# Performance work log

Hardware: AMD Instinct MI355X
Metric: run time of the kernel (lower is better)

Reference implementation:

```python
import jax, jax.numpy as jnp
import numpy as np
import math

B, S, D, H = 4, 2048, 1024, 16
DK = D // H  # 64


def setup_inputs() -> dict:
    key = jax.random.key(0)
    ks = jax.random.split(key, 8)
    sc = 1.0 / math.sqrt(D)
    Q = jax.random.normal(ks[0], (B, S, D), dtype=jnp.float32)
    K = jax.random.normal(ks[1], (B, S, D), dtype=jnp.float32)
    V = jax.random.normal(ks[2], (B, S, D), dtype=jnp.float32)
    # per-head projection weights, stacked: [H, D, DK]
    Wq = jax.random.normal(ks[3], (H, D, DK), dtype=jnp.float32) * sc
    Wk = jax.random.normal(ks[4], (H, D, DK), dtype=jnp.float32) * sc
    Wv = jax.random.normal(ks[5], (H, D, DK), dtype=jnp.float32) * sc
    Wo = jax.random.normal(ks[6], (D, D), dtype=jnp.float32) * sc
    bo = jax.random.normal(ks[7], (D,), dtype=jnp.float32) * sc
    mask = jnp.tril(jnp.ones((S, S), dtype=bool))  # causal
    return {"Q": Q, "K": K, "V": V, "mask": mask,
            "Wq": Wq, "Wk": Wk, "Wv": Wv, "Wo": Wo, "bo": bo}


def reference(Q, K, V, mask, Wq, Wk, Wv, Wo, bo):
    # batched per-head projections: [B,S,D] x [H,D,DK] -> [B,H,S,DK]
    q = jnp.einsum('bsd,hdk->bhsk', Q, Wq)
    k = jnp.einsum('bsd,hdk->bhsk', K, Wk)
    v = jnp.einsum('bsd,hdk->bhsk', V, Wv)
    # NOTE: source scales by k.shape[-1]/sqrt(d_k) = d_k/sqrt(d_k) = sqrt(d_k)
    scale = jnp.float32(DK / math.sqrt(DK))
    w = jnp.einsum('bhsk,bhtk->bhst', q, k) * scale  # [B,H,S,S]
    w = jnp.where(mask[None, None, :, :], w, jnp.float32(-jnp.inf))
    w = jax.nn.softmax(w, axis=-1)
    out = jnp.einsum('bhst,bhtk->bhsk', w, v)  # [B,H,S,DK]
    # concat heads along last dim (head order preserved): [B,S,D]
    concat = out.transpose(0, 2, 1, 3).reshape(B, S, D)
    # output projection (dropout p=0 -> identity in eval)
    return concat @ Wo.T + bo
```

## Files before the change

kernel.cpp:

```cpp
#include <hip/hip_runtime.h>
#include <math.h>


#define BB 4
#define SS 2048
#define DD 1024
#define HH 16
#define DKK 64
#define MM (BB * SS)

typedef unsigned short u16;
typedef _Float16 f16x8 __attribute__((ext_vector_type(8)));
typedef float f32x4 __attribute__((ext_vector_type(4)));
typedef __attribute__((address_space(1))) unsigned int gas_u32;
typedef __attribute__((address_space(3))) unsigned int las_u32;

__device__ __forceinline__ float bf2f(u16 u) {
    union { unsigned int i; float f; } c;
    c.i = ((unsigned int)u) << 16;
    return c.f;
}
__device__ __forceinline__ u16 f2h(float f) {
    _Float16 h = (_Float16)f;
    return __builtin_bit_cast(u16, h);
}
__device__ __forceinline__ void split1(float x, u16& hi, u16& lo) {
    _Float16 hh = (_Float16)x;
    hi = __builtin_bit_cast(u16, hh);
    lo = f2h(x - (float)hh);
}
__device__ __forceinline__ void gld16(const void* g, void* l) {
    __builtin_amdgcn_global_load_lds((gas_u32*)g, (las_u32*)l, 16, 0, 0);
}

__global__ void sniff_kernel(const u16* t0, const u16* t1, const u16* t2,
                             const u16* t3, const u16* t4, const u16* t5,
                             const u16* t6, const u16* t7, int* flags)
{
    const u16* ptrs[8] = {t0, t1, t2, t3, t4, t5, t6, t7};
    const u16* p = ptrs[blockIdx.x];
    int tid = threadIdx.x;
    int cnt = 0;
    #pragma unroll
    for (int i = 0; i < 8; i++) {
        u16 v = p[tid * 8 + i];
        int e = (v >> 7) & 0xFF;
        if (e >= 0xF0 || (e <= 0x0F && (v & 0x7FFF) != 0)) cnt++;
    }
    #pragma unroll
    for (int off = 32; off; off >>= 1) cnt += __shfl_down(cnt, off);
    if (tid == 0) flags[blockIdx.x] = (cnt >= 4) ? 1 : 0;
}

__global__ __launch_bounds__(256) void split_x_kernel(
    const void* __restrict__ X, const int* __restrict__ flags, int fidx,
    u16* __restrict__ Xh, u16* __restrict__ Xl)
{
    const int xf = flags[fidx];
    size_t idx = ((size_t)blockIdx.x * 256 + threadIdx.x) * 8;
    float x[8];
    if (xf) {
        float4 a = *(const float4*)((const float*)X + idx);
        float4 b = *(const float4*)((const float*)X + idx + 4);
        x[0] = a.x; x[1] = a.y; x[2] = a.z; x[3] = a.w;
        x[4] = b.x; x[5] = b.y; x[6] = b.z; x[7] = b.w;
    } else {
        ushort4 a = *(const ushort4*)((const u16*)X + idx);
        ushort4 b = *(const ushort4*)((const u16*)X + idx + 4);
        x[0] = bf2f(a.x); x[1] = bf2f(a.y); x[2] = bf2f(a.z); x[3] = bf2f(a.w);
        x[4] = bf2f(b.x); x[5] = bf2f(b.y); x[6] = bf2f(b.z); x[7] = bf2f(b.w);
    }
    union { u16 u[8]; uint4 v; } H, L;
    #pragma unroll
    for (int i = 0; i < 8; i++) split1(x[i], H.u[i], L.u[i]);
    *(uint4*)(Xh + idx) = H.v;
    *(uint4*)(Xl + idx) = L.v;
}

__global__ __launch_bounds__(256) void split_wqkv_kernel(
    const void* __restrict__ Wq, const void* __restrict__ Wk, const void* __restrict__ Wv,
    const int* __restrict__ flags, u16* __restrict__ Wth, u16* __restrict__ Wtl)
{
    const int z = blockIdx.z, h = blockIdx.y, kc = blockIdx.x;
    const void* __restrict__ W = (z == 0) ? Wq : (z == 1) ? Wk : Wv;
    const int wf = flags[3 + z];
    __shared__ float T[64][65];
    const int t = threadIdx.x;
    {
        const int kk = t >> 2, ns = (t & 3) * 16;
        const size_t base = (size_t)h * DD * DKK + (size_t)(kc * 64 + kk) * DKK + ns;
        #pragma unroll
        for (int j = 0; j < 4; j++) {
            if (wf) {
                float4 v = *(const float4*)((const float*)W + base + 4 * j);
                T[kk][ns + 4 * j + 0] = v.x; T[kk][ns + 4 * j + 1] = v.y;
                T[kk][ns + 4 * j + 2] = v.z; T[kk][ns + 4 * j + 3] = v.w;
            } else {
                ushort4 v = *(const ushort4*)((const u16*)W + base + 4 * j);
                T[kk][ns + 4 * j + 0] = bf2f(v.x); T[kk][ns + 4 * j + 1] = bf2f(v.y);
                T[kk][ns + 4 * j + 2] = bf2f(v.z); T[kk][ns + 4 * j + 3] = bf2f(v.w);
            }
        }
    }
    __syncthreads();
    {
        const int n = t >> 2, ks = (t & 3) * 16;
        union { u16 u[16]; uint4 v[2]; } Hv, Lv;
        #pragma unroll
        for (int i = 0; i < 16; i++) split1(T[ks + i][n], Hv.u[i], Lv.u[i]);
        size_t ob = ((size_t)(z * HH + h) * DKK + n) * DD + kc * 64 + ks;
        *(uint4*)(Wth + ob)     = Hv.v[0];
        *(uint4*)(Wth + ob + 8) = Hv.v[1];
        *(uint4*)(Wtl + ob)     = Lv.v[0];
        *(uint4*)(Wtl + ob + 8) = Lv.v[1];
    }
}

__global__ __launch_bounds__(256, 4) void proj_v4_kernel(
    const void* __restrict__ Q, const void* __restrict__ K, const void* __restrict__ V,
    const u16* __restrict__ Wth, const u16* __restrict__ Wtl,
    const int* __restrict__ flags,
    u16* __restrict__ qb, u16* __restrict__ kb, u16* __restrict__ vb)
{
    const int z = blockIdx.z;
    const void* __restrict__ X = (z == 0) ? Q : (z == 1) ? K : V;
    u16* __restrict__ out      = (z == 0) ? qb : (z == 1) ? kb : vb;
    const int xf = flags[z];
    const int h0 = blockIdx.y * 2;
    const int m0 = blockIdx.x * 128;

    __shared__ __align__(16) u16 WH[128 * 64];
    __shared__ __align__(16) u16 WL[128 * 64];

    const int tid  = threadIdx.x;
    const int lane = tid & 63, wave = tid >> 6;
    const int quad = lane >> 4, ln = lane & 15;

    const int lr = lane >> 3, lg = (lane & 7) ^ (lane >> 3);
    const size_t wsrc0 = ((size_t)((z * HH + h0) * DKK) + wave * 32 + lr) * DD + lg * 8;
    const size_t arow = (size_t)(m0 + wave * 32 + ln) * DD + quad * 8;

    f32x4 acc[2][8];
    #pragma unroll
    for (int mh = 0; mh < 2; mh++)
        #pragma unroll
        for (int nt = 0; nt < 8; nt++)
            acc[mh][nt] = (f32x4){0.f, 0.f, 0.f, 0.f};

    for (int kbase = 0; kbase < DD; kbase += 64) {
        __syncthreads();
        f16x8 a_h[2][2], a_l[2][2];
        #pragma unroll
        for (int kh = 0; kh < 2; kh++)
            #pragma unroll
            for (int mh = 0; mh < 2; mh++) {
                size_t o = arow + (size_t)(mh * 16) * DD + kbase + kh * 32;
                float x[8];
                if (xf) {
                    float4 a = *(const float4*)((const float*)X + o);
                    float4 b = *(const float4*)((const float*)X + o + 4);
                    x[0] = a.x; x[1] = a.y; x[2] = a.z; x[3] = a.w;
                    x[4] = b.x; x[5] = b.y; x[6] = b.z; x[7] = b.w;
                } else {
                    ushort4 a = *(const ushort4*)((const u16*)X + o);
                    ushort4 b = *(const ushort4*)((const u16*)X + o + 4);
                    x[0] = bf2f(a.x); x[1] = bf2f(a.y); x[2] = bf2f(a.z); x[3] = bf2f(a.w);
                    x[4] = bf2f(b.x); x[5] = bf2f(b.y); x[6] = bf2f(b.z); x[7] = bf2f(b.w);
                }
                union { u16 u[8]; f16x8 v; } H, L;
                #pragma unroll
                for (int i = 0; i < 8; i++) split1(x[i], H.u[i], L.u[i]);
                a_h[kh][mh] = H.v;
                a_l[kh][mh] = L.v;
            }
        #pragma unroll
        for (int j = 0; j < 4; j++) {
            gld16(Wth + wsrc0 + (size_t)j * 8 * DD + kbase, &WH[(wave * 32 + j * 8) * 64]);
            gld16(Wtl + wsrc0 + (size_t)j * 8 * DD + kbase, &WL[(wave * 32 + j * 8) * 64]);
        }
        asm volatile("s_waitcnt vmcnt(0)" ::: "memory");
        __syncthreads();

        #pragma unroll
        for (int kh = 0; kh < 2; kh++) {
            const int kg = ((kh * 4 + quad) ^ (ln & 7)) * 8;
            #pragma unroll
            for (int nt = 0; nt < 8; nt++) {
                const int n = nt * 16 + ln;
                f16x8 bh = __builtin_bit_cast(f16x8, *(const uint4*)&WH[n * 64 + kg]);
                f16x8 bl = __builtin_bit_cast(f16x8, *(const uint4*)&WL[n * 64 + kg]);
                #pragma unroll
                for (int mh = 0; mh < 2; mh++) {
                    acc[mh][nt] = __builtin_amdgcn_mfma_f32_16x16x32_f16(a_l[kh][mh], bh, acc[mh][nt], 0, 0, 0);
                    acc[mh][nt] = __builtin_amdgcn_mfma_f32_16x16x32_f16(a_h[kh][mh], bl, acc[mh][nt], 0, 0, 0);
                    acc[mh][nt] = __builtin_amdgcn_mfma_f32_16x16x32_f16(a_h[kh][mh], bh, acc[mh][nt], 0, 0, 0);
                }
            }
        }
    }

    #pragma unroll
    for (int mh = 0; mh < 2; mh++)
        #pragma unroll
        for (int r = 0; r < 4; r++) {
            int m = m0 + wave * 32 + mh * 16 + quad * 4 + r;
            int b = m >> 11, s = m & 2047;
            #pragma unroll
            for (int nt = 0; nt < 8; nt++) {
                int head = h0 + (nt >> 2);
                u16* op = out + (((size_t)(b * HH + head) * SS + s)) * DKK;
                op[(nt & 3) * 16 + ln] = f2h(acc[mh][nt][r]);
            }
        }
}

__global__ __launch_bounds__(512) void attn_kernel(
    const u16* __restrict__ qb, const u16* __restrict__ kb,
    const u16* __restrict__ vb, u16* __restrict__ cath, u16* __restrict__ catl)
{
    __shared__ __align__(16) u16 Kt[2][64 * 64];
    __shared__ __align__(16) u16 Vt[2][64 * 64];
    __shared__ __align__(16) u16 Pw[8][16 * 64];

    const int tid  = threadIdx.x;
    const int lane = tid & 63, wave = tid >> 6;
    const int quad = lane >> 4, ln = lane & 15;

    const int p  = blockIdx.x;
    const int bh = (p >> 6) * 8 + (p & 7);
    const int pairidx = (p >> 3) & 7;
    const int b = bh >> 4, h = bh & 15;

    const int skey = tid >> 3, kgrp = tid & 7;
    const int koff = skey * 64 + ((kgrp ^ (skey & 7)) << 3);
    const int vkey = tid & 63, vdkb = (tid >> 6) * 8;

    const u16* kbp = kb + (size_t)bh * SS * DKK;
    const u16* vbp = vb + (size_t)bh * SS * DKK;

    #pragma unroll 1
    for (int half = 0; half < 2; half++) {
        const int xt = half == 0 ? 15 - pairidx : pairidx;
        const int qbase = xt * 128;
        const int ktmax = 2 * xt + 1;

        const int wq = qbase + wave * 16;
        const int diagkt = wq >> 6;
        const int wqmax = wq + 15;

        const u16* qp = qb + ((size_t)bh * SS + wq + ln) * DKK;
        f16x8 qf0 = __builtin_bit_cast(f16x8, *(const uint4*)(qp + quad * 8));
        f16x8 qf1 = __builtin_bit_cast(f16x8, *(const uint4*)(qp + 32 + quad * 8));

        f32x4 acc[4];
        #pragma unroll
        for (int n = 0; n < 4; n++) acc[n] = (f32x4){0.f, 0.f, 0.f, 0.f};
        float mrow[4], lrow[4];
        #pragma unroll
        for (int r = 0; r < 4; r++) { mrow[r] = -INFINITY; lrow[r] = 0.f; }

        {
            uint4 ka = *(const uint4*)(kbp + (size_t)skey * DKK + kgrp * 8);
            uint4 va = *(const uint4*)(vbp + (size_t)vkey * DKK + vdkb);
            *(uint4*)&Kt[0][koff] = ka;
            u16 vv[8];
            *(uint4*)&vv[0] = va;
            #pragma unroll
            for (int i = 0; i < 8; i++) {
                int row = vdkb + i;
                Vt[0][row * 64 + (((vkey >> 3) ^ (row & 7)) << 3) + (vkey & 7)] = vv[i];
            }
        }
        __syncthreads();

        int cur = 0;
        for (int kt = 0; kt <= ktmax; ++kt) {
            uint4 ka, va;
            const bool pfb = (kt < ktmax);
            if (pfb) {
                ka = *(const uint4*)(kbp + (size_t)((kt + 1) * 64 + skey) * DKK + kgrp * 8);
                va = *(const uint4*)(vbp + (size_t)((kt + 1) * 64 + vkey) * DKK + vdkb);
            }

            if (kt * 64 <= wqmax) {
                const u16* KT = Kt[cur];
                const u16* VT = Vt[cur];
                f32x4 sa[4];
                #pragma unroll
                for (int n = 0; n < 4; n++) {
                    sa[n] = (f32x4){0.f, 0.f, 0.f, 0.f};
                    const int krow = n * 16 + ln;
                    f16x8 kf0 = __builtin_bit_cast(f16x8,
                        *(const uint4*)&KT[krow * 64 + ((quad ^ (ln & 7)) << 3)]);
                    sa[n] = __builtin_amdgcn_mfma_f32_16x16x32_f16(qf0, kf0, sa[n], 0, 0, 0);
                    f16x8 kf1 = __builtin_bit_cast(f16x8,
                        *(const uint4*)&KT[krow * 64 + (((quad + 4) ^ (ln & 7)) << 3)]);
                    sa[n] = __builtin_amdgcn_mfma_f32_16x16x32_f16(qf1, kf1, sa[n], 0, 0, 0);
                }

                float sc[4][4];
                const bool diag = (kt == diagkt);
                #pragma unroll
                for (int n = 0; n < 4; n++)
                    #pragma unroll
                    for (int r = 0; r < 4; r++) {
                        float s = sa[n][r] * 8.0f;
                        if (diag && (kt * 64 + n * 16 + ln) > (wq + quad * 4 + r))
                            s = -INFINITY;
                        sc[n][r] = s;
                    }

                float rmax[4];
                #pragma unroll
                for (int r = 0; r < 4; r++)
                    rmax[r] = fmaxf(fmaxf(sc[0][r], sc[1][r]), fmaxf(sc[2][r], sc[3][r]));
                #pragma unroll
                for (int off = 1; off < 16; off <<= 1)
                    #pragma unroll
                    for (int r = 0; r < 4; r++)
                        rmax[r] = fmaxf(rmax[r], __shfl_xor(rmax[r], off));
                float alpha[4];
                #pragma unroll
                for (int r = 0; r < 4; r++) {
                    float mn = fmaxf(mrow[r], rmax[r]);
                    alpha[r] = __expf(mrow[r] - mn);
                    mrow[r] = mn;
                }
                u16* pw = Pw[wave];
                float lsum[4] = {0.f, 0.f, 0.f, 0.f};
                #pragma unroll
                for (int n = 0; n < 4; n++)
                    #pragma unroll
                    for (int r = 0; r < 4; r++) {
                        float pp = __expf(sc[n][r] - mrow[r]);
                        _Float16 ph = (_Float16)pp;
                        const int row = quad * 4 + r;
                        pw[row * 64 + (((n * 2 + (ln >> 3)) ^ (row & 7)) << 3) + (ln & 7)]
                            = __builtin_bit_cast(u16, ph);
                        lsum[r] += (float)ph;
                    }
                #pragma unroll
                for (int off = 1; off < 16; off <<= 1)
                    #pragma unroll
                    for (int r = 0; r < 4; r++)
                        lsum[r] += __shfl_xor(lsum[r], off);
                #pragma unroll
                for (int r = 0; r < 4; r++)
                    lrow[r] = lrow[r] * alpha[r] + lsum[r];
                #pragma unroll
                for (int n = 0; n < 4; n++)
                    #pragma unroll
                    for (int r = 0; r < 4; r++)
                        acc[n][r] *= alpha[r];

                asm volatile("s_waitcnt lgkmcnt(0)" ::: "memory");
                f16x8 pf0 = __builtin_bit_cast(f16x8,
                    *(const uint4*)&pw[ln * 64 + ((quad ^ (ln & 7)) << 3)]);
                f16x8 pf1 = __builtin_bit_cast(f16x8,
                    *(const uint4*)&pw[ln * 64 + (((quad + 4) ^ (ln & 7)) << 3)]);

                #pragma unroll
                for (int n = 0; n < 4; n++) {
                    const int vrow = n * 16 + ln;
                    f16x8 vf0 = __builtin_bit_cast(f16x8,
                        *(const uint4*)&VT[vrow * 64 + ((quad ^ (ln & 7)) << 3)]);
                    acc[n] = __builtin_amdgcn_mfma_f32_16x16x32_f16(pf0, vf0, acc[n], 0, 0, 0);
                    f16x8 vf1 = __builtin_bit_cast(f16x8,
                        *(const uint4*)&VT[vrow * 64 + (((quad + 4) ^ (ln & 7)) << 3)]);
                    acc[n] = __builtin_amdgcn_mfma_f32_16x16x32_f16(pf1, vf1, acc[n], 0, 0, 0);
                }
            }

            if (pfb) {
                *(uint4*)&Kt[cur ^ 1][koff] = ka;
                u16 vv[8];
                *(uint4*)&vv[0] = va;
                #pragma unroll
                for (int i = 0; i < 8; i++) {
                    int row = vdkb + i;
                    Vt[cur ^ 1][row * 64 + (((vkey >> 3) ^ (row & 7)) << 3) + (vkey & 7)] = vv[i];
                }
            }
            __syncthreads();
            cur ^= 1;
        }

        #pragma unroll
        for (int r = 0; r < 4; r++) {
            float inv = 1.0f / lrow[r];
            int row = wq + quad * 4 + r;
            size_t o = ((size_t)b * SS + row) * DD + h * DKK;
            #pragma unroll
            for (int n = 0; n < 4; n++) {
                float v = acc[n][r] * inv;
                u16 hh, ll;
                split1(v, hh, ll);
                cath[o + n * 16 + ln] = hh;
                catl[o + n * 16 + ln] = ll;
            }
        }
    }
}

__global__ __launch_bounds__(256, 4) void outproj_v3_kernel(
    const u16* __restrict__ Ah, const u16* __restrict__ Al,
    const u16* __restrict__ Woh, const u16* __restrict__ Wol,
    const void* __restrict__ bo, const int* __restrict__ flags,
    float* __restrict__ out)
{
    const int n0 = blockIdx.y * 128;
    const int m0 = blockIdx.x * 128;

    __shared__ __align__(16) u16 WH[128 * 64];
    __shared__ __align__(16) u16 WL[128 * 64];

    const int tid  = threadIdx.x;
    const int lane = tid & 63, wave = tid >> 6;
    const int quad = lane >> 4, ln = lane & 15;

    const int lr = lane >> 3, lg = (lane & 7) ^ (lane >> 3);
    const size_t wsrc0 = ((size_t)(n0 + wave * 32 + lr)) * DD + lg * 8;
    const size_t arow  = (size_t)(m0 + wave * 32 + ln) * DD + quad * 8;

    f32x4 acc[2][8];
    #pragma unroll
    for (int mh = 0; mh < 2; mh++)
        #pragma unroll
        for (int nt = 0; nt < 8; nt++)
            acc[mh][nt] = (f32x4){0.f, 0.f, 0.f, 0.f};

    for (int kbase = 0; kbase < DD; kbase += 64) {
        __syncthreads();
        f16x8 a_h[2][2], a_l[2][2];
        #pragma unroll
        for (int kh = 0; kh < 2; kh++)
            #pragma unroll
            for (int mh = 0; mh < 2; mh++) {
                size_t o = arow + (size_t)(mh * 16) * DD + kbase + kh * 32;
                a_h[kh][mh] = __builtin_bit_cast(f16x8, *(const uint4*)(Ah + o));
                a_l[kh][mh] = __builtin_bit_cast(f16x8, *(const uint4*)(Al + o));
            }
        #pragma unroll
        for (int j = 0; j < 4; j++) {
            gld16(Woh + wsrc0 + (size_t)j * 8 * DD + kbase, &WH[(wave * 32 + j * 8) * 64]);
            gld16(Wol + wsrc0 + (size_t)j * 8 * DD + kbase, &WL[(wave * 32 + j * 8) * 64]);
        }
        asm volatile("s_waitcnt vmcnt(0)" ::: "memory");
        __syncthreads();

        #pragma unroll
        for (int kh = 0; kh < 2; kh++) {
            const int kg = ((kh * 4 + quad) ^ (ln & 7)) * 8;
            #pragma unroll
            for (int nt = 0; nt < 8; nt++) {
                const int n = nt * 16 + ln;
                f16x8 bh = __builtin_bit_cast(f16x8, *(const uint4*)&WH[n * 64 + kg]);
                f16x8 bl = __builtin_bit_cast(f16x8, *(const uint4*)&WL[n * 64 + kg]);
                #pragma unroll
                for (int mh = 0; mh < 2; mh++) {
                    acc[mh][nt] = __builtin_amdgcn_mfma_f32_16x16x32_f16(a_l[kh][mh], bh, acc[mh][nt], 0, 0, 0);
                    acc[mh][nt] = __builtin_amdgcn_mfma_f32_16x16x32_f16(a_h[kh][mh], bl, acc[mh][nt], 0, 0, 0);
                    acc[mh][nt] = __builtin_amdgcn_mfma_f32_16x16x32_f16(a_h[kh][mh], bh, acc[mh][nt], 0, 0, 0);
                }
            }
        }
    }

    const int bf = flags[7];
    float bias[8];
    #pragma unroll
    for (int nt = 0; nt < 8; nt++) {
        int n = n0 + nt * 16 + ln;
        bias[nt] = bf ? ((const float*)bo)[n] : bf2f(((const u16*)bo)[n]);
    }
    #pragma unroll
    for (int mh = 0; mh < 2; mh++)
        #pragma unroll
        for (int r = 0; r < 4; r++) {
            int m = m0 + wave * 32 + mh * 16 + quad * 4 + r;
            float* op = out + (size_t)m * DD + n0;
            #pragma unroll
            for (int nt = 0; nt < 8; nt++)
                op[nt * 16 + ln] = acc[mh][nt][r] + bias[nt];
        }
}

extern "C" void kernel_launch(void* const* d_in, const int* in_sizes, int n_in,
                              void* d_out, int out_size, void* d_ws, size_t ws_size,
                              hipStream_t stream)
{
    const void* Q = d_in[0];
    const void* K = d_in[1];
    const void* V = d_in[2];
    const int widx = (n_in >= 9) ? 4 : 3;
    const void* Wq = d_in[widx + 0];
    const void* Wk = d_in[widx + 1];
    const void* Wv = d_in[widx + 2];
    const void* Wo = d_in[widx + 3];
    const void* bo = d_in[widx + 4];
    float* out = (float*)d_out;

    const size_t per = (size_t)BB * HH * SS * DKK;
    u16* qb = (u16*)d_ws;
    u16* kb = qb + per;
    u16* vb = kb + per;
    u16* cath = vb + per;
    u16* catl = cath + per;
    const size_t wtn = (size_t)3 * HH * DKK * DD;
    u16* Wth = catl + per;
    u16* Wtl = Wth + wtn;
    u16* Woh = Wtl + wtn;
    u16* Wol = Woh + (size_t)DD * DD;
    int* flags = (int*)(Wol + (size_t)DD * DD);

    sniff_kernel<<<8, 64, 0, stream>>>(
        (const u16*)Q, (const u16*)K, (const u16*)V,
        (const u16*)Wq, (const u16*)Wk, (const u16*)Wv,
        (const u16*)Wo, (const u16*)bo, flags);

    split_wqkv_kernel<<<dim3(DD / 64, HH, 3), 256, 0, stream>>>(
        Wq, Wk, Wv, flags, Wth, Wtl);
    split_x_kernel<<<(DD * DD) / 2048, 256, 0, stream>>>(Wo, flags, 6, Woh, Wol);

    proj_v4_kernel<<<dim3(MM / 128, HH / 2, 3), 256, 0, stream>>>(
        Q, K, V, Wth, Wtl, flags, qb, kb, vb);

    attn_kernel<<<(SS / 256) * BB * HH, 512, 0, stream>>>(qb, kb, vb, cath, catl);

    outproj_v3_kernel<<<dim3(MM / 128, DD / 128), 256, 0, stream>>>(
        cath, catl, Woh, Wol, bo, flags, out);
}
```

Measured before the change: 470.6 us.

## Double-buffer weight tiles and prefetch A operands in projection GEMMs

The QKV projection and output projection kernels now use double-buffered LDS tiles for the weight halves. The next k-step's A-operand global loads and weight async copies are issued before the current step's MFMA work, so memory latency overlaps with compute. The MFMA section runs at raised wave priority via s_setprio. LDS use per block doubles and launch bounds drop to 2 blocks per CU. That lowers occupancy and adds register pressure from the prefetched A registers.

Result: no change. 478.9 us (+1.8%).

```diff
diff --git a/kernel.cpp b/kernel.cpp
--- a/kernel.cpp
+++ b/kernel.cpp
@@ -116,7 +116,7 @@
     }
 }
 
-__global__ __launch_bounds__(256, 4) void proj_v4_kernel(
+__global__ __launch_bounds__(256, 2) void proj_v5_kernel(
     const void* __restrict__ Q, const void* __restrict__ K, const void* __restrict__ V,
     const u16* __restrict__ Wth, const u16* __restrict__ Wtl,
     const int* __restrict__ flags,
@@ -129,8 +129,8 @@
     const int h0 = blockIdx.y * 2;
     const int m0 = blockIdx.x * 128;
 
-    __shared__ __align__(16) u16 WH[128 * 64];
-    __shared__ __align__(16) u16 WL[128 * 64];
+    __shared__ __align__(16) u16 WH[2][128 * 64];
+    __shared__ __align__(16) u16 WL[2][128 * 64];
 
     const int tid  = threadIdx.x;
     const int lane = tid & 63, wave = tid >> 6;
@@ -147,25 +147,38 @@
         for (int nt = 0; nt < 8; nt++)
             acc[mh][nt] = (f32x4){0.f, 0.f, 0.f, 0.f};
 
-    for (int kbase = 0; kbase < DD; kbase += 64) {
-        __syncthreads();
-        f16x8 a_h[2][2], a_l[2][2];
+    uint4 ra[2][2], rb[2][2];
+    f16x8 a_h[2][2], a_l[2][2];
+
+    auto issueA = [&](int kbase) {
         #pragma unroll
         for (int kh = 0; kh < 2; kh++)
             #pragma unroll
             for (int mh = 0; mh < 2; mh++) {
                 size_t o = arow + (size_t)(mh * 16) * DD + kbase + kh * 32;
+                if (xf) {
+                    ra[kh][mh] = *(const uint4*)((const float*)X + o);
+                    rb[kh][mh] = *(const uint4*)((const float*)X + o + 4);
+                } else {
+                    ra[kh][mh] = *(const uint4*)((const u16*)X + o);
+                }
+            }
+    };
+    auto splitA = [&]() {
+        #pragma unroll
+        for (int kh = 0; kh < 2; kh++)
+            #pragma unroll
+            for (int mh = 0; mh < 2; mh++) {
                 float x[8];
                 if (xf) {
-                    float4 a = *(const float4*)((const float*)X + o);
-                    float4 b = *(const float4*)((const float*)X + o + 4);
+                    float4 a = __builtin_bit_cast(float4, ra[kh][mh]);
+                    float4 b = __builtin_bit_cast(float4, rb[kh][mh]);
                     x[0] = a.x; x[1] = a.y; x[2] = a.z; x[3] = a.w;
                     x[4] = b.x; x[5] = b.y; x[6] = b.z; x[7] = b.w;
                 } else {
-                    ushort4 a = *(const ushort4*)((const u16*)X + o);
-                    ushort4 b = *(const ushort4*)((const u16*)X + o + 4);
-                    x[0] = bf2f(a.x); x[1] = bf2f(a.y); x[2] = bf2f(a.z); x[3] = bf2f(a.w);
-                    x[4] = bf2f(b.x); x[5] = bf2f(b.y); x[6] = bf2f(b.z); x[7] = bf2f(b.w);
+                    union { uint4 v; u16 u[8]; } c; c.v = ra[kh][mh];
+                    #pragma unroll
+                    for (int i = 0; i < 8; i++) x[i] = bf2f(c.u[i]);
                 }
                 union { u16 u[8]; f16x8 v; } H, L;
                 #pragma unroll
@@ -173,22 +186,37 @@
                 a_h[kh][mh] = H.v;
                 a_l[kh][mh] = L.v;
             }
+    };
+    auto issueW = [&](int kbase, int c) {
         #pragma unroll
         for (int j = 0; j < 4; j++) {
-            gld16(Wth + wsrc0 + (size_t)j * 8 * DD + kbase, &WH[(wave * 32 + j * 8) * 64]);
-            gld16(Wtl + wsrc0 + (size_t)j * 8 * DD + kbase, &WL[(wave * 32 + j * 8) * 64]);
-        }
-        asm volatile("s_waitcnt vmcnt(0)" ::: "memory");
-        __syncthreads();
-
+            gld16(Wth + wsrc0 + (size_t)j * 8 * DD + kbase, &WH[c][(wave * 32 + j * 8) * 64]);
+            gld16(Wtl + wsrc0 + (size_t)j * 8 * DD + kbase, &WL[c][(wave * 32 + j * 8) * 64]);
+        }
+    };
+
+    issueA(0);
+    issueW(0, 0);
+    splitA();
+    asm volatile("s_waitcnt vmcnt(0)" ::: "memory");
+    __syncthreads();
+
+    int c = 0;
+    for (int k = 0; k < 16; ++k) {
+        const bool notlast = (k < 15);
+        if (notlast) {
+            issueA((k + 1) * 64);
+            issueW((k + 1) * 64, c ^ 1);
+        }
+        __builtin_amdgcn_s_setprio(1);
         #pragma unroll
         for (int kh = 0; kh < 2; kh++) {
             const int kg = ((kh * 4 + quad) ^ (ln & 7)) * 8;
             #pragma unroll
             for (int nt = 0; nt < 8; nt++) {
                 const int n = nt * 16 + ln;
-                f16x8 bh = __builtin_bit_cast(f16x8, *(const uint4*)&WH[n * 64 + kg]);
-                f16x8 bl = __builtin_bit_cast(f16x8, *(const uint4*)&WL[n * 64 + kg]);
+                f16x8 bh = __builtin_bit_cast(f16x8, *(const uint4*)&WH[c][n * 64 + kg]);
+                f16x8 bl = __builtin_bit_cast(f16x8, *(const uint4*)&WL[c][n * 64 + kg]);
                 #pragma unroll
                 for (int mh = 0; mh < 2; mh++) {
                     acc[mh][nt] = __builtin_amdgcn_mfma_f32_16x16x32_f16(a_l[kh][mh], bh, acc[mh][nt], 0, 0, 0);
@@ -197,6 +225,13 @@
                 }
             }
         }
+        __builtin_amdgcn_s_setprio(0);
+        if (notlast) {
+            splitA();
+            asm volatile("s_waitcnt vmcnt(0)" ::: "memory");
+            __syncthreads();
+        }
+        c ^= 1;
     }
 
     #pragma unroll
@@ -402,7 +437,7 @@
     }
 }
 
-__global__ __launch_bounds__(256, 4) void outproj_v3_kernel(
+__global__ __launch_bounds__(256, 2) void outproj_v4_kernel(
     const u16* __restrict__ Ah, const u16* __restrict__ Al,
     const u16* __restrict__ Woh, const u16* __restrict__ Wol,
     const void* __restrict__ bo, const int* __restrict__ flags,
@@ -411,8 +446,8 @@
     const int n0 = blockIdx.y * 128;
     const int m0 = blockIdx.x * 128;
 
-    __shared__ __align__(16) u16 WH[128 * 64];
-    __shared__ __align__(16) u16 WL[128 * 64];
+    __shared__ __align__(16) u16 WH[2][128 * 64];
+    __shared__ __align__(16) u16 WL[2][128 * 64];
 
     const int tid  = threadIdx.x;
     const int lane = tid & 63, wave = tid >> 6;
@@ -429,33 +464,58 @@
         for (int nt = 0; nt < 8; nt++)
             acc[mh][nt] = (f32x4){0.f, 0.f, 0.f, 0.f};
 
-    for (int kbase = 0; kbase < DD; kbase += 64) {
-        __syncthreads();
-        f16x8 a_h[2][2], a_l[2][2];
+    uint4 rh[2][2], rl[2][2];
+    f16x8 a_h[2][2], a_l[2][2];
+
+    auto issueA = [&](int kbase) {
         #pragma unroll
         for (int kh = 0; kh < 2; kh++)
             #pragma unroll
             for (int mh = 0; mh < 2; mh++) {
                 size_t o = arow + (size_t)(mh * 16) * DD + kbase + kh * 32;
-                a_h[kh][mh] = __builtin_bit_cast(f16x8, *(const uint4*)(Ah + o));
-                a_l[kh][mh] = __builtin_bit_cast(f16x8, *(const uint4*)(Al + o));
-            }
+                rh[kh][mh] = *(const uint4*)(Ah + o);
+                rl[kh][mh] = *(const uint4*)(Al + o);
+            }
+    };
+    auto takeA = [&]() {
+        #pragma unroll
+        for (int kh = 0; kh < 2; kh++)
+            #pragma unroll
+            for (int mh = 0; mh < 2; mh++) {
+                a_h[kh][mh] = __builtin_bit_cast(f16x8, rh[kh][mh]);
+                a_l[kh][mh] = __builtin_bit_cast(f16x8, rl[kh][mh]);
+            }
+    };
+    auto issueW = [&](int kbase, int c) {
         #pragma unroll
         for (int j = 0; j < 4; j++) {
-            gld16(Woh + wsrc0 + (size_t)j * 8 * DD + kbase, &WH[(wave * 32 + j * 8) * 64]);
-            gld16(Wol + wsrc0 + (size_t)j * 8 * DD + kbase, &WL[(wave * 32 + j * 8) * 64]);
-        }
-        asm volatile("s_waitcnt vmcnt(0)" ::: "memory");
-        __syncthreads();
-
+            gld16(Woh + wsrc0 + (size_t)j * 8 * DD + kbase, &WH[c][(wave * 32 + j * 8) * 64]);
+            gld16(Wol + wsrc0 + (size_t)j * 8 * DD + kbase, &WL[c][(wave * 32 + j * 8) * 64]);
+        }
+    };
+
+    issueA(0);
+    issueW(0, 0);
+    takeA();
+    asm volatile("s_waitcnt vmcnt(0)" ::: "memory");
+    __syncthreads();
+
+    int c = 0;
+    for (int k = 0; k < 16; ++k) {
+        const bool notlast = (k < 15);
+        if (notlast) {
+            issueA((k + 1) * 64);
+            issueW((k + 1) * 64, c ^ 1);
+        }
+        __builtin_amdgcn_s_setprio(1);
         #pragma unroll
         for (int kh = 0; kh < 2; kh++) {
             const int kg = ((kh * 4 + quad) ^ (ln & 7)) * 8;
             #pragma unroll
             for (int nt = 0; nt < 8; nt++) {
                 const int n = nt * 16 + ln;
-                f16x8 bh = __builtin_bit_cast(f16x8, *(const uint4*)&WH[n * 64 + kg]);
-                f16x8 bl = __builtin_bit_cast(f16x8, *(const uint4*)&WL[n * 64 + kg]);
+                f16x8 bh = __builtin_bit_cast(f16x8, *(const uint4*)&WH[c][n * 64 + kg]);
+                f16x8 bl = __builtin_bit_cast(f16x8, *(const uint4*)&WL[c][n * 64 + kg]);
                 #pragma unroll
                 for (int mh = 0; mh < 2; mh++) {
                     acc[mh][nt] = __builtin_amdgcn_mfma_f32_16x16x32_f16(a_l[kh][mh], bh, acc[mh][nt], 0, 0, 0);
@@ -464,6 +524,13 @@
                 }
             }
         }
+        __builtin_amdgcn_s_setprio(0);
+        if (notlast) {
+            takeA();
+            asm volatile("s_waitcnt vmcnt(0)" ::: "memory");
+            __syncthreads();
+        }
+        c ^= 1;
     }
 
     const int bf = flags[7];
@@ -522,11 +589,11 @@
         Wq, Wk, Wv, flags, Wth, Wtl);
     split_x_kernel<<<(DD * DD) / 2048, 256, 0, stream>>>(Wo, flags, 6, Woh, Wol);
 
-    proj_v4_kernel<<<dim3(MM / 128, HH / 2, 3), 256, 0, stream>>>(
+    proj_v5_kernel<<<dim3(MM / 128, HH / 2, 3), 256, 0, stream>>>(
         Q, K, V, Wth, Wtl, flags, qb, kb, vb);
 
     attn_kernel<<<(SS / 256) * BB * HH, 512, 0, stream>>>(qb, kb, vb, cath, catl);
 
-    outproj_v3_kernel<<<dim3(MM / 128, DD / 128), 256, 0, stream>>>(
+    outproj_v4_kernel<<<dim3(MM / 128, DD / 128), 256, 0, stream>>>(
         cath, catl, Woh, Wol, bo, flags, out);
 }
```
